# Optimization experiments

Hardware: AMD Instinct MI355X
Metric: run time of the kernel (lower is better)

## Reference

```python
import jax, jax.numpy as jnp
import numpy as np

DIM, HEADS, DHEAD, CTX_DIM, DFF = 1280, 20, 64, 768, 5120
EPS = 1e-5
SCALE = DHEAD ** -0.5


def layer_norm(x, g, b):
    mu = jnp.mean(x, axis=-1, keepdims=True)
    var = jnp.mean(jnp.square(x - mu), axis=-1, keepdims=True)
    return (x - mu) * jax.lax.rsqrt(var + EPS) * g + b


def cross_attention(x, ctx, wq, wk, wv, wo, bo):
    B, N, _ = x.shape
    M = ctx.shape[1]
    q = jnp.einsum('bne,ef->bnf', x, wq).reshape(B, N, HEADS, DHEAD).transpose(0, 2, 1, 3)
    k = jnp.einsum('bme,ef->bmf', ctx, wk).reshape(B, M, HEADS, DHEAD).transpose(0, 2, 1, 3)
    v = jnp.einsum('bme,ef->bmf', ctx, wv).reshape(B, M, HEADS, DHEAD).transpose(0, 2, 1, 3)
    scores = jnp.einsum('bhnd,bhmd->bhnm', q, k) * SCALE
    attn = jax.nn.softmax(scores, axis=-1)
    out = jnp.einsum('bhnm,bhmd->bhnd', attn, v)
    out = out.transpose(0, 2, 1, 3).reshape(B, N, HEADS * DHEAD)
    return jnp.einsum('bnf,fe->bne', out, wo) + bo


def geglu_ff(x, w1, b1, w2, b2):
    h = jnp.einsum('bne,ef->bnf', x, w1) + b1  # [B,N,2*DFF]
    a, gate = h[..., :DFF], h[..., DFF:]
    h = a * jax.nn.gelu(gate)
    return jnp.einsum('bnf,fe->bne', h, w2) + b2


def block_forward(x, context,
                  g1, be1, wq1, wk1, wv1, wo1, bo1,
                  g2, be2, wq2, wk2, wv2, wo2, bo2,
                  g3, be3, w_ff1, b_ff1, w_ff2, b_ff2):
    x = cross_attention(layer_norm(x, g1, be1), layer_norm(x, g1, be1), wq1, wk1, wv1, wo1, bo1) + x
    x = cross_attention(layer_norm(x, g2, be2), context, wq2, wk2, wv2, wo2, bo2) + x
    return geglu_ff(layer_norm(x, g3, be3), w_ff1, b_ff1, w_ff2, b_ff2) + x


def setup_inputs() -> dict:
    key = jax.random.key(0)
    ks = jax.random.split(key, 20)
    s = 0.02
    inner = HEADS * DHEAD
    return {
        'x': jax.random.normal(ks[0], (4, 1024, DIM), jnp.float32),
        'context': jax.random.normal(ks[1], (4, 77, CTX_DIM), jnp.float32),
        'g1': jnp.ones((DIM,), jnp.float32), 'be1': jnp.zeros((DIM,), jnp.float32),
        'wq1': jax.random.normal(ks[2], (DIM, inner), jnp.float32) * s,
        'wk1': jax.random.normal(ks[3], (DIM, inner), jnp.float32) * s,
        'wv1': jax.random.normal(ks[4], (DIM, inner), jnp.float32) * s,
        'wo1': jax.random.normal(ks[5], (inner, DIM), jnp.float32) * s,
        'bo1': jnp.zeros((DIM,), jnp.float32),
        'g2': jnp.ones((DIM,), jnp.float32), 'be2': jnp.zeros((DIM,), jnp.float32),
        'wq2': jax.random.normal(ks[6], (DIM, inner), jnp.float32) * s,
        'wk2': jax.random.normal(ks[7], (CTX_DIM, inner), jnp.float32) * s,
        'wv2': jax.random.normal(ks[8], (CTX_DIM, inner), jnp.float32) * s,
        'wo2': jax.random.normal(ks[9], (inner, DIM), jnp.float32) * s,
        'bo2': jnp.zeros((DIM,), jnp.float32),
        'g3': jnp.ones((DIM,), jnp.float32), 'be3': jnp.zeros((DIM,), jnp.float32),
        'w_ff1': jax.random.normal(ks[10], (DIM, 2 * DFF), jnp.float32) * s,
        'b_ff1': jnp.zeros((2 * DFF,), jnp.float32),
        'w_ff2': jax.random.normal(ks[11], (DFF, DIM), jnp.float32) * s,
        'b_ff2': jnp.zeros((DIM,), jnp.float32),
    }


def reference(x, context,
              g1, be1, wq1, wk1, wv1, wo1, bo1,
              g2, be2, wq2, wk2, wv2, wo2, bo2,
              g3, be3, w_ff1, b_ff1, w_ff2, b_ff2):
    return block_forward(x, context,
                         g1, be1, wq1, wk1, wv1, wo1, bo1,
                         g2, be2, wq2, wk2, wv2, wo2, bo2,
                         g3, be3, w_ff1, b_ff1, w_ff2, b_ff2)
```

## Files before the change

### kernel.cpp

```cpp
#include <hip/hip_runtime.h>

typedef unsigned short u16;
typedef __bf16 bf16x8 __attribute__((ext_vector_type(8)));
typedef float f32x4 __attribute__((ext_vector_type(4)));

static __device__ __forceinline__ float bf2f(u16 u) {
    union { unsigned int i; float f; } v; v.i = ((unsigned int)u) << 16; return v.f;
}
static __device__ __forceinline__ u16 f2bf(float f) {
    union { float f; unsigned int i; } v; v.f = f;
    unsigned int b = v.i;
    b += 0x7fffu + ((b >> 16) & 1u);
    return (u16)(b >> 16);
}
static __device__ __forceinline__ u16 ldbf(const void* p, size_t i, int isf32) {
    return isf32 ? f2bf(((const float*)p)[i]) : ((const u16*)p)[i];
}
static __device__ __forceinline__ float ldf(const void* p, size_t i, int isf32) {
    return isf32 ? ((const float*)p)[i] : bf2f(((const u16*)p)[i]);
}
static __device__ __forceinline__ void glds16(const u16* g, u16* l) {
    __builtin_amdgcn_global_load_lds(
        (const __attribute__((address_space(1))) unsigned int*)g,
        (__attribute__((address_space(3))) unsigned int*)l,
        16, 0, 0);
}
static __device__ __forceinline__ int xcd_swz(int lid, int nwg) {
    return ((nwg & 7) == 0) ? ((lid & 7) * (nwg >> 3) + (lid >> 3)) : lid;
}

__global__ __launch_bounds__(256) void k_detect(const u16* __restrict__ xu, int* __restrict__ flag) {
    u16 v = xu[threadIdx.x * 2];
    int e = (v >> 7) & 0xFF;
    int sane = (e >= 87 && e <= 133) ? 1 : 0;
    int total = __syncthreads_count(sane);
    if (threadIdx.x == 0) flag[0] = (total < 192) ? 1 : 0;
}

__global__ __launch_bounds__(256) void k_b2f(const void* __restrict__ in, float* __restrict__ out, int n,
                                             const int* __restrict__ flagp) {
    int isf32 = *flagp;
    int i = blockIdx.x * 256 + threadIdx.x;
    if (i < n) out[i] = ldf(in, i, isf32);
}

__global__ __launch_bounds__(256) void k_cvt(const void* __restrict__ in, u16* __restrict__ out, int n,
                                             const int* __restrict__ flagp) {
    int isf32 = *flagp;
    int i = blockIdx.x * 256 + threadIdx.x;
    if (i < n) out[i] = ldbf(in, i, isf32);
}

__global__ __launch_bounds__(256) void k_addp(float* __restrict__ X, const float* __restrict__ P, int n4) {
    int i = blockIdx.x * 256 + threadIdx.x;
    int stride = gridDim.x * 256;
    for (; i < n4; i += stride) {
        f32x4 a = ((const f32x4*)X)[i];
        f32x4 b = ((const f32x4*)P)[i];
        a[0] += b[0]; a[1] += b[1]; a[2] += b[2]; a[3] += b[3];
        ((f32x4*)X)[i] = a;
    }
}

__global__ __launch_bounds__(256) void k_transpose(const void* __restrict__ W, u16* __restrict__ Wt,
                                                   int K, int N, const int* __restrict__ flagp) {
    int isf32 = *flagp;
    __shared__ u16 T[32][33];
    int k0 = blockIdx.x * 32, n0 = blockIdx.y * 32;
    int tid = threadIdx.x;
    int c = tid & 31, rr = tid >> 5;
    #pragma unroll
    for (int j = 0; j < 4; ++j) {
        int k = rr + j * 8;
        T[k][c] = ldbf(W, (size_t)(k0 + k) * N + n0 + c, isf32);
    }
    __syncthreads();
    #pragma unroll
    for (int j = 0; j < 4; ++j) {
        int n = rr + j * 8;
        Wt[(size_t)(n0 + n) * K + k0 + c] = T[c][n];
    }
}

__global__ __launch_bounds__(256) void k_transpose3(const void* __restrict__ W0, const void* __restrict__ W1,
                                                    const void* __restrict__ W2,
                                                    u16* __restrict__ D0, u16* __restrict__ D1,
                                                    u16* __restrict__ D2,
                                                    int K, int N, const int* __restrict__ flagp) {
    int isf32 = *flagp;
    int z = blockIdx.z;
    const void* W = (z == 0) ? W0 : (z == 1) ? W1 : W2;
    u16* Wt = (z == 0) ? D0 : (z == 1) ? D1 : D2;
    __shared__ u16 T[32][33];
    int k0 = blockIdx.x * 32, n0 = blockIdx.y * 32;
    int tid = threadIdx.x;
    int c = tid & 31, rr = tid >> 5;
    #pragma unroll
    for (int j = 0; j < 4; ++j) {
        int k = rr + j * 8;
        T[k][c] = ldbf(W, (size_t)(k0 + k) * N + n0 + c, isf32);
    }
    __syncthreads();
    #pragma unroll
    for (int j = 0; j < 4; ++j) {
        int n = rr + j * 8;
        Wt[(size_t)(n0 + n) * K + k0 + c] = T[c][n];
    }
}

__global__ __launch_bounds__(256) void k_layernorm(float* __restrict__ X, const float* __restrict__ P,
                                                   const void* __restrict__ G, const void* __restrict__ Bb,
                                                   u16* __restrict__ Y, int D,
                                                   const int* __restrict__ flagp) {
    int isf32 = *flagp;
    int row = blockIdx.x;
    float* xr = X + (size_t)row * D;
    const float* pr = P ? (P + (size_t)row * D) : nullptr;
    float s = 0.f, s2 = 0.f;
    for (int i = threadIdx.x; i < D; i += 256) {
        float v = xr[i] + (P ? pr[i] : 0.f);
        s += v; s2 += v * v;
    }
    #pragma unroll
    for (int off = 32; off; off >>= 1) { s += __shfl_down(s, off); s2 += __shfl_down(s2, off); }
    __shared__ float rs[4], rs2[4];
    __shared__ float stat[2];
    int w = threadIdx.x >> 6;
    if ((threadIdx.x & 63) == 0) { rs[w] = s; rs2[w] = s2; }
    __syncthreads();
    if (threadIdx.x == 0) {
        float ts = rs[0] + rs[1] + rs[2] + rs[3];
        float ts2 = rs2[0] + rs2[1] + rs2[2] + rs2[3];
        float mu = ts / D;
        float var = ts2 / D - mu * mu;
        stat[0] = mu; stat[1] = rsqrtf(var + 1e-5f);
    }
    __syncthreads();
    float mu = stat[0], rstd = stat[1];
    u16* yr = Y + (size_t)row * D;
    for (int i = threadIdx.x; i < D; i += 256) {
        float v = xr[i] + (P ? pr[i] : 0.f);
        if (P) xr[i] = v;
        yr[i] = f2bf((v - mu) * rstd * ldf(G, i, isf32) + ldf(Bb, i, isf32));
    }
}

template <int EPI>
__global__ __launch_bounds__(512, 2) void k_gemm8(const u16* __restrict__ A, const u16* __restrict__ Bt,
                                                  void* __restrict__ Cout, const void* __restrict__ bias,
                                                  int M, int N, int K, const int* __restrict__ flagp) {
    __shared__ __align__(16) u16 sm[65536];
    const int tid = threadIdx.x;
    const int w = tid >> 6;
    const int lane = tid & 63;
    const int quad = lane >> 4, r = lane & 15;
    const int wm = w >> 2, wn = w & 3;
    const int lid = blockIdx.x + blockIdx.y * gridDim.x;
    const int nid = xcd_swz(lid, gridDim.x * gridDim.y);
    const int row0 = (nid % gridDim.x) * 256;
    const int col0 = (nid / gridDim.x) * 256;
    const int NT = K >> 6;

    const u16* aP[2][2];
    const u16* bP[2][2];
    #pragma unroll
    for (int j = 0; j < 2; ++j) {
        int c = tid + w * 64 + j * 64;
        int rj = c >> 3;
        int qe = (c & 7) ^ (rj & 7);
        #pragma unroll
        for (int h = 0; h < 2; ++h) {
            int gr = h * 128 + rj;
            aP[h][j] = A + (size_t)(row0 + gr) * K + qe * 8;
            int n = col0 + gr;
            int m = (EPI == 1) ? (((n >> 4) & 1) * 5120 + (n >> 5) * 16 + (n & 15)) : n;
            bP[h][j] = Bt + (size_t)m * K + qe * 8;
        }
    }
    auto stageA = [&](int h, int t) {
        u16* base = sm + (t & 1) * 32768 + h * 8192 + w * 1024;
        glds16(aP[h][0] + t * 64, base);
        glds16(aP[h][1] + t * 64, base + 512);
    };
    auto stageB = [&](int h, int t) {
        u16* base = sm + (t & 1) * 32768 + 16384 + h * 8192 + w * 1024;
        glds16(bP[h][0] + t * 64, base);
        glds16(bP[h][1] + t * 64, base + 512);
    };

    f32x4 acc[2][2][4][2] = {};
    const int xq = r & 7;
    bf16x8 afA[4][2], afB[4][2], bf0[2][2], bf1[2][2];

    auto readA = [&](bf16x8 (&dst)[4][2], int Ab, int half) {
        #pragma unroll
        for (int i = 0; i < 4; ++i) {
            int ar = half * 128 + wm * 64 + i * 16 + r;
            #pragma unroll
            for (int ks = 0; ks < 2; ++ks)
                dst[i][ks] = *(const bf16x8*)(sm + Ab + ar * 64 + (((ks * 4 + quad) ^ xq) * 8));
        }
    };
    auto readB = [&](bf16x8 (&dst)[2][2], int Bb, int half) {
        #pragma unroll
        for (int g = 0; g < 2; ++g) {
            int br = half * 128 + wn * 32 + g * 16 + r;
            #pragma unroll
            for (int ks = 0; ks < 2; ++ks)
                dst[g][ks] = *(const bf16x8*)(sm + Bb + br * 64 + (((ks * 4 + quad) ^ xq) * 8));
        }
    };
    auto domfma = [&](int qm, int qn, bf16x8 (&a)[4][2], bf16x8 (&b)[2][2]) {
        #pragma unroll
        for (int ks = 0; ks < 2; ++ks)
            #pragma unroll
            for (int i = 0; i < 4; ++i)
                #pragma unroll
                for (int g = 0; g < 2; ++g)
                    acc[qm][qn][i][g] = __builtin_amdgcn_mfma_f32_16x16x32_bf16(
                        a[i][ks], b[g][ks], acc[qm][qn][i][g], 0, 0, 0);
    };

    stageA(0, 0); stageB(0, 0); stageA(1, 0); stageB(1, 0);
    if (NT > 1) {
        stageA(0, 1); stageB(0, 1);
        asm volatile("s_waitcnt vmcnt(4)" ::: "memory");
    } else {
        asm volatile("s_waitcnt vmcnt(0)" ::: "memory");
    }
    __builtin_amdgcn_s_barrier();
    readA(afA, 0, 0);
    readB(bf0, 16384, 0);

    for (int t = 0; t < NT; ++t) {
        const int Ab = (t & 1) * 32768;
        const int Bb = Ab + 16384;
        const int Abn = ((t + 1) & 1) * 32768;
        readB(bf1, Bb, 1);
        __builtin_amdgcn_sched_barrier(0);
        __builtin_amdgcn_s_setprio(1);
        domfma(0, 0, afA, bf0);
        __builtin_amdgcn_s_setprio(0);
        if (t + 1 < NT) stageA(1, t + 1);
        __builtin_amdgcn_s_barrier();
        readA(afB, Ab, 1);
        __builtin_amdgcn_sched_barrier(0);
        __builtin_amdgcn_s_setprio(1);
        domfma(0, 1, afA, bf1);
        __builtin_amdgcn_s_setprio(0);
        if (t + 1 < NT) stageB(1, t + 1);
        __builtin_amdgcn_s_barrier();
        __builtin_amdgcn_s_setprio(1);
        domfma(1, 1, afB, bf1);
        __builtin_amdgcn_s_setprio(0);
        if (t + 2 < NT) stageA(0, t + 2);
        __builtin_amdgcn_s_barrier();
        __builtin_amdgcn_s_setprio(1);
        domfma(1, 0, afB, bf0);
        __builtin_amdgcn_s_setprio(0);
        if (t + 2 < NT) stageB(0, t + 2);
        if (t + 2 < NT) asm volatile("s_waitcnt vmcnt(4)" ::: "memory");
        else            asm volatile("s_waitcnt vmcnt(0)" ::: "memory");
        __builtin_amdgcn_s_barrier();
        if (t + 1 < NT) {
            readA(afA, Abn, 0);
            readB(bf0, Abn + 16384, 0);
        }
    }

    if (EPI == 0) {
        u16* C = (u16*)Cout;
        #pragma unroll
        for (int qm = 0; qm < 2; ++qm) {
            #pragma unroll
            for (int qn = 0; qn < 2; ++qn) {
                #pragma unroll
                for (int i = 0; i < 4; ++i) {
                    int grow = row0 + qm * 128 + wm * 64 + i * 16 + quad * 4;
                    #pragma unroll
                    for (int g = 0; g < 2; ++g) {
                        int gcol = col0 + qn * 128 + wn * 32 + g * 16 + r;
                        #pragma unroll
                        for (int t4 = 0; t4 < 4; ++t4)
                            C[(size_t)(grow + t4) * N + gcol] = f2bf(acc[qm][qn][i][g][t4]);
                    }
                }
            }
        }
    } else {
        const int isf32 = *flagp;
        u16* C = (u16*)Cout;
        #pragma unroll
        for (int qm = 0; qm < 2; ++qm) {
            #pragma unroll
            for (int qn = 0; qn < 2; ++qn) {
                int ncb = col0 + qn * 128 + wn * 32;
                int oc = (ncb >> 1) + r;
                float bva = ldf(bias, oc, isf32);
                float bvu = ldf(bias, 5120 + oc, isf32);
                #pragma unroll
                for (int i = 0; i < 4; ++i) {
                    int grow = row0 + qm * 128 + wm * 64 + i * 16 + quad * 4;
                    #pragma unroll
                    for (int t4 = 0; t4 < 4; ++t4) {
                        float a = acc[qm][qn][i][0][t4] + bva;
                        float u = acc[qm][qn][i][1][t4] + bvu;
                        float z2 = 1.5957691216f * (u + 0.044715f * u * u * u);
                        float gl = u * __builtin_amdgcn_rcpf(1.f + __expf(-z2));
                        C[(size_t)(grow + t4) * 5120 + oc] = f2bf(a * gl);
                    }
                }
            }
        }
    }
}

template <int EPI>
__global__ __launch_bounds__(256) void k_gemm_t(const u16* __restrict__ A, const u16* __restrict__ Bt,
                                                void* __restrict__ Cout, float* __restrict__ Rf,
                                                const void* __restrict__ bias,
                                                int M, int N, int K, const int* __restrict__ flagp) {
    int isf32 = *flagp;
    __shared__ __align__(16) u16 As[4096];
    __shared__ __align__(16) u16 Bs[4096];
    int tid = threadIdx.x;
    int row0 = blockIdx.x * 128, col0 = blockIdx.y * 128;
    int S = gridDim.z, kz = blockIdx.z;
    int kseg = K / S;
    int kb = kz * kseg, ke = kb + kseg;
    int wave = tid >> 6, lane = tid & 63;
    int wm = (wave >> 1) * 64, wn = (wave & 1) * 64;
    int quad = lane >> 4, r = lane & 15;
    int c0 = wave * 64 + lane, c1 = 256 + c0;
    int ar0 = c0 >> 2, aq0 = (c0 & 3) ^ ((ar0 >> 1) & 3);
    int ar1 = c1 >> 2, aq1 = (c1 & 3) ^ ((ar1 >> 1) & 3);
    const u16* Ag0 = A + (size_t)min(row0 + ar0, M - 1) * K + aq0 * 8;
    const u16* Ag1 = A + (size_t)min(row0 + ar1, M - 1) * K + aq1 * 8;
    const u16* Bg0 = Bt + (size_t)(col0 + ar0) * K + aq0 * 8;
    const u16* Bg1 = Bt + (size_t)(col0 + ar1) * K + aq1 * 8;
    u16* lA0 = As + wave * 512;
    u16* lA1 = As + 2048 + wave * 512;
    u16* lB0 = Bs + wave * 512;
    u16* lB1 = Bs + 2048 + wave * 512;
    f32x4 acc[4][4] = {};
    for (int k0 = kb; k0 < ke; k0 += 32) {
        __syncthreads();
        glds16(Ag0 + k0, lA0);
        glds16(Ag1 + k0, lA1);
        glds16(Bg0 + k0, lB0);
        glds16(Bg1 + k0, lB1);
        __syncthreads();
        bf16x8 af[4], bfv[4];
        #pragma unroll
        for (int i = 0; i < 4; ++i) {
            int row = wm + i * 16 + r;
            af[i] = *(const bf16x8*)(As + (row * 4 + (quad ^ ((row >> 1) & 3))) * 8);
        }
        #pragma unroll
        for (int g = 0; g < 4; ++g) {
            int row = wn + g * 16 + r;
            bfv[g] = *(const bf16x8*)(Bs + (row * 4 + (quad ^ ((row >> 1) & 3))) * 8);
        }
        #pragma unroll
        for (int i = 0; i < 4; ++i)
            #pragma unroll
            for (int g = 0; g < 4; ++g)
                acc[i][g] = __builtin_amdgcn_mfma_f32_16x16x32_bf16(af[i], bfv[g], acc[i][g], 0, 0, 0);
    }
    #pragma unroll
    for (int i = 0; i < 4; ++i) {
        int grow = row0 + wm + i * 16 + quad * 4;
        if (grow >= M) continue;
        #pragma unroll
        for (int g = 0; g < 4; ++g) {
            int gcol = col0 + wn + g * 16 + r;
            float bv = (EPI == 2 && kz == 0) ? ldf(bias, gcol, isf32) : 0.f;
            #pragma unroll
            for (int t = 0; t < 4; ++t) {
                float v = acc[i][g][t];
                size_t off = (size_t)(grow + t) * N + gcol;
                if (EPI == 0) {
                    ((u16*)Cout)[off] = f2bf(v);
                } else {
                    if (kz == 0) Rf[off] += v + bv;
                    else         ((float*)Cout)[off] = v;
                }
            }
        }
    }
}

__global__ __launch_bounds__(256) void k_geglu_t(const u16* __restrict__ A, const u16* __restrict__ Bt,
                                                 const void* __restrict__ bias, u16* __restrict__ Out,
                                                 int M, int K, const int* __restrict__ flagp) {
    const int Nout = 5120;
    int isf32 = *flagp;
    __shared__ __align__(16) u16 As[4096];
    __shared__ __align__(16) u16 Bs[4096];
    int tid = threadIdx.x;
    int row0 = blockIdx.x * 128, col0 = blockIdx.y * 64;
    int wave = tid >> 6, lane = tid & 63;
    int quad = lane >> 4, r = lane & 15;
    int c0 = wave * 64 + lane, c1 = 256 + c0;
    int ar0 = c0 >> 2, aq0 = (c0 & 3) ^ ((ar0 >> 1) & 3);
    int ar1 = c1 >> 2, aq1 = (c1 & 3) ^ ((ar1 >> 1) & 3);
    const u16* Ag0 = A + (size_t)min(row0 + ar0, M - 1) * K + aq0 * 8;
    const u16* Ag1 = A + (size_t)min(row0 + ar1, M - 1) * K + aq1 * 8;
    const u16* Bg0 = Bt + (size_t)((ar0 >> 6) * Nout + col0 + (ar0 & 63)) * K + aq0 * 8;
    const u16* Bg1 = Bt + (size_t)((ar1 >> 6) * Nout + col0 + (ar1 & 63)) * K + aq1 * 8;
    u16* lA0 = As + wave * 512;
    u16* lA1 = As + 2048 + wave * 512;
    u16* lB0 = Bs + wave * 512;
    u16* lB1 = Bs + 2048 + wave * 512;
    f32x4 acc[2][2][4] = {};
    for (int k0 = 0; k0 < K; k0 += 32) {
        __syncthreads();
        glds16(Ag0 + k0, lA0);
        glds16(Ag1 + k0, lA1);
        glds16(Bg0 + k0, lB0);
        glds16(Bg1 + k0, lB1);
        __syncthreads();
        bf16x8 af[2], bv[2][4];
        #pragma unroll
        for (int i = 0; i < 2; ++i) {
            int row = wave * 32 + i * 16 + r;
            af[i] = *(const bf16x8*)(As + (row * 4 + (quad ^ ((row >> 1) & 3))) * 8);
        }
        #pragma unroll
        for (int p = 0; p < 2; ++p)
            #pragma unroll
            for (int g = 0; g < 4; ++g) {
                int row = p * 64 + g * 16 + r;
                bv[p][g] = *(const bf16x8*)(Bs + (row * 4 + (quad ^ ((row >> 1) & 3))) * 8);
            }
        #pragma unroll
        for (int p = 0; p < 2; ++p)
            #pragma unroll
            for (int i = 0; i < 2; ++i)
                #pragma unroll
                for (int g = 0; g < 4; ++g)
                    acc[p][i][g] = __builtin_amdgcn_mfma_f32_16x16x32_bf16(af[i], bv[p][g], acc[p][i][g], 0, 0, 0);
    }
    #pragma unroll
    for (int i = 0; i < 2; ++i) {
        int grow = row0 + wave * 32 + i * 16 + quad * 4;
        #pragma unroll
        for (int g = 0; g < 4; ++g) {
            int gcol = col0 + g * 16 + r;
            float bva = ldf(bias, gcol, isf32);
            float bvu = ldf(bias, Nout + gcol, isf32);
            #pragma unroll
            for (int t = 0; t < 4; ++t) {
                float a = acc[0][i][g][t] + bva;
                float u = acc[1][i][g][t] + bvu;
                float z2 = 1.5957691216f * (u + 0.044715f * u * u * u);
                float gl = u * __builtin_amdgcn_rcpf(1.f + __expf(-z2));
                Out[(size_t)(grow + t) * Nout + gcol] = f2bf(a * gl);
            }
        }
    }
}

template <int EPI, bool AEXT>
__global__ __launch_bounds__(256) void k_gemm(const void* __restrict__ A, const void* __restrict__ B,
                                              void* __restrict__ Cout, float* __restrict__ Rf,
                                              const void* __restrict__ bias,
                                              int M, int N, int K, const int* __restrict__ flagp) {
    int isf32 = *flagp;
    __shared__ u16 As[64][40];
    __shared__ u16 Bs[64][40];
    int tid = threadIdx.x;
    int row0 = blockIdx.x * 64, col0 = blockIdx.y * 64;
    int wave = tid >> 6, lane = tid & 63;
    int wm = (wave >> 1) * 32, wn = (wave & 1) * 32;
    int quad = lane >> 4, r = lane & 15;
    int arow = tid >> 2, akk = (tid & 3) * 8;
    int bnl = tid & 63, bkk = (tid >> 6) * 8;
    int garow = row0 + arow;
    f32x4 acc[2][2] = {};
    for (int k0 = 0; k0 < K; k0 += 32) {
        uint4 aval = {0u, 0u, 0u, 0u};
        if (garow < M) {
            if (AEXT && isf32) {
                const float* Af = (const float*)A;
                u16 t[8];
                #pragma unroll
                for (int j = 0; j < 8; ++j) t[j] = f2bf(Af[(size_t)garow * K + k0 + akk + j]);
                aval = *(uint4*)t;
            } else {
                aval = *(const uint4*)((const u16*)A + (size_t)garow * K + k0 + akk);
            }
        }
        u16 btmp[8];
        #pragma unroll
        for (int j = 0; j < 8; ++j) btmp[j] = ldbf(B, (size_t)(k0 + bkk + j) * N + col0 + bnl, isf32);
        __syncthreads();
        *(uint4*)(&As[arow][akk]) = aval;
        *(uint4*)(&Bs[bnl][bkk]) = *(uint4*)btmp;
        __syncthreads();
        bf16x8 a0 = *(const bf16x8*)(&As[wm + r][quad * 8]);
        bf16x8 a1 = *(const bf16x8*)(&As[wm + 16 + r][quad * 8]);
        bf16x8 b0 = *(const bf16x8*)(&Bs[wn + r][quad * 8]);
        bf16x8 b1 = *(const bf16x8*)(&Bs[wn + 16 + r][quad * 8]);
        acc[0][0] = __builtin_amdgcn_mfma_f32_16x16x32_bf16(a0, b0, acc[0][0], 0, 0, 0);
        acc[0][1] = __builtin_amdgcn_mfma_f32_16x16x32_bf16(a0, b1, acc[0][1], 0, 0, 0);
        acc[1][0] = __builtin_amdgcn_mfma_f32_16x16x32_bf16(a1, b0, acc[1][0], 0, 0, 0);
        acc[1][1] = __builtin_amdgcn_mfma_f32_16x16x32_bf16(a1, b1, acc[1][1], 0, 0, 0);
    }
    #pragma unroll
    for (int i = 0; i < 2; ++i)
        #pragma unroll
        for (int jn = 0; jn < 2; ++jn)
            #pragma unroll
            for (int t = 0; t < 4; ++t) {
                int grow = row0 + wm + i * 16 + quad * 4 + t;
                int gcol = col0 + wn + jn * 16 + r;
                if (grow >= M) continue;
                float v = acc[i][jn][t];
                size_t off = (size_t)grow * N + gcol;
                if (EPI == 0) {
                    ((u16*)Cout)[off] = f2bf(v);
                } else if (EPI == 2) {
                    Rf[off] += v + ldf(bias, gcol, isf32);
                } else {
                    ((float*)Cout)[off] = v + ldf(bias, gcol, isf32) + Rf[off];
                }
            }
}

__global__ __launch_bounds__(256) void k_gemm_geglu(const u16* __restrict__ A, const void* __restrict__ B,
                                                    const void* __restrict__ bias, u16* __restrict__ Out,
                                                    int M, int Nout, int K, int ldb,
                                                    const int* __restrict__ flagp) {
    int isf32 = *flagp;
    __shared__ u16 As[64][40];
    __shared__ u16 Bs[64][40];
    int tid = threadIdx.x;
    int row0 = blockIdx.x * 64, col0 = blockIdx.y * 64;
    int wave = tid >> 6, lane = tid & 63;
    int wm = (wave >> 1) * 32, wn = (wave & 1) * 32;
    int quad = lane >> 4, r = lane & 15;
    int arow = tid >> 2, akk = (tid & 3) * 8;
    int bnl = tid & 63, bkk = (tid >> 6) * 8;
    int garow = row0 + arow;
    f32x4 acc[2][2][2] = {};
    for (int p = 0; p < 2; ++p) {
        for (int k0 = 0; k0 < K; k0 += 32) {
            uint4 aval = {0u, 0u, 0u, 0u};
            if (garow < M) aval = *(const uint4*)(A + (size_t)garow * K + k0 + akk);
            u16 btmp[8];
            #pragma unroll
            for (int j = 0; j < 8; ++j)
                btmp[j] = ldbf(B, (size_t)(k0 + bkk + j) * ldb + p * Nout + col0 + bnl, isf32);
            __syncthreads();
            *(uint4*)(&As[arow][akk]) = aval;
            *(uint4*)(&Bs[bnl][bkk]) = *(uint4*)btmp;
            __syncthreads();
            bf16x8 a0 = *(const bf16x8*)(&As[wm + r][quad * 8]);
            bf16x8 a1 = *(const bf16x8*)(&As[wm + 16 + r][quad * 8]);
            bf16x8 b0 = *(const bf16x8*)(&Bs[wn + r][quad * 8]);
            bf16x8 b1 = *(const bf16x8*)(&Bs[wn + 16 + r][quad * 8]);
            acc[p][0][0] = __builtin_amdgcn_mfma_f32_16x16x32_bf16(a0, b0, acc[p][0][0], 0, 0, 0);
            acc[p][0][1] = __builtin_amdgcn_mfma_f32_16x16x32_bf16(a0, b1, acc[p][0][1], 0, 0, 0);
            acc[p][1][0] = __builtin_amdgcn_mfma_f32_16x16x32_bf16(a1, b0, acc[p][1][0], 0, 0, 0);
            acc[p][1][1] = __builtin_amdgcn_mfma_f32_16x16x32_bf16(a1, b1, acc[p][1][1], 0, 0, 0);
        }
    }
    #pragma unroll
    for (int i = 0; i < 2; ++i)
        #pragma unroll
        for (int jn = 0; jn < 2; ++jn)
            #pragma unroll
            for (int t = 0; t < 4; ++t) {
                int grow = row0 + wm + i * 16 + quad * 4 + t;
                int gcol = col0 + wn + jn * 16 + r;
                if (grow >= M) continue;
                float a = acc[0][i][jn][t] + ldf(bias, gcol, isf32);
                float u = acc[1][i][jn][t] + ldf(bias, Nout + gcol, isf32);
                float th = tanhf(0.7978845608f * (u + 0.044715f * u * u * u));
                float gl = 0.5f * u * (1.f + th);
                Out[(size_t)grow * Nout + gcol] = f2bf(a * gl);
            }
}

__global__ __launch_bounds__(256) void k_attn_flash(const u16* __restrict__ Q, const u16* __restrict__ K,
                                                    const u16* __restrict__ V, u16* __restrict__ O,
                                                    int N, int Mkv, int H, int ldq, int ldkv, int ldo) {
    __shared__ u16 KT[64][72];
    __shared__ u16 VT[64][72];
    __shared__ u16 Sp[4][16][72];
    const float SC = 0.18033688f;
    int nt = N / 64;
    int qt = blockIdx.x % nt;
    int bh = blockIdx.x / nt;
    int h = bh % H, b = bh / H;
    int tid = threadIdx.x, wave = tid >> 6, lane = tid & 63;
    int quad = lane >> 4, r = lane & 15;
    int q0 = qt * 64 + wave * 16;

    const u16* qbase = Q + ((size_t)(b * N + q0 + r)) * ldq + h * 64;
    bf16x8 aq0 = *(const bf16x8*)(qbase + quad * 8);
    bf16x8 aq1 = *(const bf16x8*)(qbase + 32 + quad * 8);

    f32x4 accO[4] = {};
    float m_i = -1e30f, l_i = 0.f;

    int srow = tid >> 2;
    int scol = (tid & 3) * 8;

    for (int kv0 = 0; kv0 < Mkv; kv0 += 64) {
        int krow = min(kv0 + srow, Mkv - 1);
        const u16* kp = K + ((size_t)(b * Mkv + krow)) * ldkv + h * 64;
        const u16* vp = V + ((size_t)(b * Mkv + krow)) * ldkv + h * 64;
        uint4 ka = *(const uint4*)(kp + scol);
        uint4 kb = *(const uint4*)(kp + scol + 32);
        uint4 va = *(const uint4*)(vp + scol);
        uint4 vb = *(const uint4*)(vp + scol + 32);

        __syncthreads();
        *(uint4*)(&KT[srow][scol]) = ka;
        *(uint4*)(&KT[srow][scol + 32]) = kb;
        u16 tmp[16];
        *(uint4*)tmp = va; *(uint4*)(tmp + 8) = vb;
        #pragma unroll
        for (int j = 0; j < 8; ++j) {
            VT[scol + j][srow] = tmp[j];
            VT[scol + 32 + j][srow] = tmp[8 + j];
        }
        __syncthreads();

        bf16x8 bk[4][2];
        #pragma unroll
        for (int g = 0; g < 4; ++g) {
            bk[g][0] = *(const bf16x8*)(&KT[g * 16 + r][quad * 8]);
            bk[g][1] = *(const bf16x8*)(&KT[g * 16 + r][32 + quad * 8]);
        }
        f32x4 s[4] = {};
        #pragma unroll
        for (int g = 0; g < 4; ++g) {
            s[g] = __builtin_amdgcn_mfma_f32_16x16x32_bf16(bk[g][0], aq0, s[g], 0, 0, 0);
            s[g] = __builtin_amdgcn_mfma_f32_16x16x32_bf16(bk[g][1], aq1, s[g], 0, 0, 0);
        }

        float v[4][4];
        float vmax = -1e30f;
        #pragma unroll
        for (int g = 0; g < 4; ++g)
            #pragma unroll
            for (int t = 0; t < 4; ++t) {
                int kvi = kv0 + g * 16 + quad * 4 + t;
                v[g][t] = (kvi < Mkv) ? s[g][t] * SC : -1e30f;
                vmax = fmaxf(vmax, v[g][t]);
            }
        vmax = fmaxf(vmax, __shfl_xor(vmax, 16));
        vmax = fmaxf(vmax, __shfl_xor(vmax, 32));
        float mn = fmaxf(m_i, vmax);
        float alpha = exp2f(m_i - mn);
        float ps = 0.f;
        #pragma unroll
        for (int g = 0; g < 4; ++g)
            #pragma unroll
            for (int t = 0; t < 4; ++t) {
                v[g][t] = exp2f(v[g][t] - mn);
                ps += v[g][t];
            }
        ps += __shfl_xor(ps, 16);
        ps += __shfl_xor(ps, 32);
        l_i = l_i * alpha + ps;
        m_i = mn;
        #pragma unroll
        for (int t = 0; t < 4; ++t) {
            float art = __shfl(alpha, quad * 4 + t);
            accO[0][t] *= art; accO[1][t] *= art; accO[2][t] *= art; accO[3][t] *= art;
        }
        #pragma unroll
        for (int g = 0; g < 4; ++g)
            #pragma unroll
            for (int t = 0; t < 4; ++t)
                Sp[wave][r][g * 16 + quad * 4 + t] = f2bf(v[g][t]);

        bf16x8 ap0 = *(const bf16x8*)(&Sp[wave][r][quad * 8]);
        bf16x8 ap1 = *(const bf16x8*)(&Sp[wave][r][32 + quad * 8]);
        #pragma unroll
        for (int g = 0; g < 4; ++g) {
            bf16x8 bv0 = *(const bf16x8*)(&VT[g * 16 + r][quad * 8]);
            bf16x8 bv1 = *(const bf16x8*)(&VT[g * 16 + r][32 + quad * 8]);
            accO[g] = __builtin_amdgcn_mfma_f32_16x16x32_bf16(ap0, bv0, accO[g], 0, 0, 0);
            accO[g] = __builtin_amdgcn_mfma_f32_16x16x32_bf16(ap1, bv1, accO[g], 0, 0, 0);
        }
    }

    u16* ob = O + ((size_t)(b * N + q0)) * ldo + h * 64;
    #pragma unroll
    for (int t = 0; t < 4; ++t) {
        float lr = __shfl(l_i, quad * 4 + t);
        float inv = 1.f / lr;
        #pragma unroll
        for (int g = 0; g < 4; ++g)
            ob[(size_t)(quad * 4 + t) * ldo + g * 16 + r] = f2bf(accO[g][t] * inv);
    }
}

extern "C" void kernel_launch(void* const* d_in, const int* in_sizes, int n_in,
                              void* d_out, int out_size, void* d_ws, size_t ws_size,
                              hipStream_t stream) {
    const void* x    = d_in[0];
    const void* ctx  = d_in[1];
    const void* g1   = d_in[2];
    const void* be1  = d_in[3];
    const void* wq1  = d_in[4];
    const void* wk1  = d_in[5];
    const void* wv1  = d_in[6];
    const void* wo1  = d_in[7];
    const void* bo1  = d_in[8];
    const void* g2   = d_in[9];
    const void* be2  = d_in[10];
    const void* wq2  = d_in[11];
    const void* wk2  = d_in[12];
    const void* wv2  = d_in[13];
    const void* wo2  = d_in[14];
    const void* bo2  = d_in[15];
    const void* g3   = d_in[16];
    const void* be3  = d_in[17];
    const void* wff1 = d_in[18];
    const void* bff1 = d_in[19];
    const void* wff2 = d_in[20];
    const void* bff2 = d_in[21];

    const int BT = 4096, D = 1280;
    dim3 blk(256);
    char* ws = (char*)d_ws;

    const size_t NEED_FAST = 117393664;
    if (ws_size >= NEED_FAST) {
        int*   flag   = (int*)(ws);
        u16* lnout    = (u16*)(ws + 256);
        u16* qkv      = (u16*)(ws + 10486016);
        u16* attnout  = (u16*)(ws + 10486016 + 31457280);
        u16* gbuf     = (u16*)(ws + 10486016);
        u16* ctxb     = (u16*)(ws + 52429056);
        u16* kv2      = (u16*)(ws + 52902144);
        u16* wqkv1t   = (u16*)(ws + 54479104);
        u16* wo1t     = (u16*)(ws + 64309504);
        u16* wq2t     = (u16*)(ws + 67586304);
        u16* wkv2t    = (u16*)(ws + 70863104);
        u16* wo2t     = (u16*)(ws + 74795264);
        u16* wff1t    = (u16*)(ws + 78072064);
        u16* wff2t    = (u16*)(ws + 104286464);
        float* pff2   = (float*)(ws + 54479104);
        float* pWO    = (float*)(ws + 10486016);
        float* xres   = (float*)d_out;

        k_detect<<<dim3(1), blk, 0, stream>>>((const u16*)x, flag);
        k_b2f<<<dim3((BT * D + 255) / 256), blk, 0, stream>>>(x, xres, BT * D, flag);
        k_transpose3<<<dim3(40, 40, 3), blk, 0, stream>>>(wq1, wk1, wv1,
                                                          wqkv1t, wqkv1t + 1280 * 1280,
                                                          wqkv1t + 2 * 1280 * 1280, 1280, 1280, flag);
        k_transpose3<<<dim3(40, 40, 3), blk, 0, stream>>>(wo1, wq2, wo2,
                                                          wo1t, wq2t, wo2t, 1280, 1280, flag);
        k_transpose3<<<dim3(24, 40, 2), blk, 0, stream>>>(wk2, wv2, wv2,
                                                          wkv2t, wkv2t + 1280 * 768,
                                                          wkv2t + 1280 * 768, 768, 1280, flag);
        k_transpose<<<dim3(40, 320), blk, 0, stream>>>(wff1, wff1t, 1280, 10240, flag);
        k_transpose<<<dim3(160, 40), blk, 0, stream>>>(wff2, wff2t, 5120, 1280, flag);
        k_cvt<<<dim3((308 * 768 + 255) / 256), blk, 0, stream>>>(ctx, ctxb, 308 * 768, flag);
        k_layernorm<<<dim3(BT), blk, 0, stream>>>(xres, nullptr, g1, be1, lnout, D, flag);
        k_gemm8<0><<<dim3(16, 15), dim3(512), 0, stream>>>(lnout, wqkv1t, qkv, nullptr, BT, 3840, D, flag);
        k_attn_flash<<<dim3(16 * 80), blk, 0, stream>>>(qkv, qkv + 1280, qkv + 2560, attnout,
                                                        1024, 1024, 20, 3840, 3840, 1280);
        k_gemm_t<2><<<dim3(32, 10, 2), blk, 0, stream>>>(attnout, wo1t, pWO, xres, bo1, BT, D, D, flag);
        k_layernorm<<<dim3(BT), blk, 0, stream>>>(xres, pWO, g2, be2, lnout, D, flag);
        k_gemm_t<0><<<dim3(32, 10), blk, 0, stream>>>(lnout, wq2t, qkv, nullptr, nullptr, BT, D, D, flag);
        k_gemm_t<0><<<dim3(3, 20), blk, 0, stream>>>(ctxb, wkv2t, kv2, nullptr, nullptr, 308, 2560, 768, flag);
        k_attn_flash<<<dim3(16 * 80), blk, 0, stream>>>(qkv, kv2, kv2 + 1280, attnout,
                                                        1024, 77, 20, 1280, 2560, 1280);
        k_gemm_t<2><<<dim3(32, 10, 2), blk, 0, stream>>>(attnout, wo2t, pWO, xres, bo2, BT, D, D, flag);
        k_layernorm<<<dim3(BT), blk, 0, stream>>>(xres, pWO, g3, be3, lnout, D, flag);
        k_gemm8<1><<<dim3(16, 40), dim3(512), 0, stream>>>(lnout, wff1t, gbuf, bff1, BT, 10240, D, flag);
        k_gemm_t<2><<<dim3(32, 10, 2), blk, 0, stream>>>(gbuf, wff2t, pff2, xres, bff2, BT, D, 5120, flag);
        k_addp<<<dim3(2048), blk, 0, stream>>>(xres, pff2, BT * D / 4);
    } else {
        int*   flag    = (int*)(ws);
        float* xres    = (float*)(ws + 256);
        u16* lnout     = (u16*)(ws + 20971776);
        u16* q         = (u16*)(ws + 31457536);
        u16* kbuf      = (u16*)(ws + 41943296);
        u16* vbuf      = (u16*)(ws + 52429056);
        u16* attnout   = (u16*)(ws + 62914816);
        u16* k2        = (u16*)(ws + 73400576);
        u16* v2        = (u16*)(ws + 74189056);
        u16* gbuf      = (u16*)(ws + 31457536);

        dim3 g_gemm(64, 20);
        dim3 g_kv(5, 20);
        dim3 g_attn(16 * 80);

        k_detect<<<dim3(1), blk, 0, stream>>>((const u16*)x, flag);
        k_b2f<<<dim3((BT * D + 255) / 256), blk, 0, stream>>>(x, xres, BT * D, flag);
        k_layernorm<<<dim3(BT), blk, 0, stream>>>(xres, nullptr, g1, be1, lnout, D, flag);
        k_gemm<0, false><<<g_gemm, blk, 0, stream>>>(lnout, wq1, q, nullptr, nullptr, BT, D, D, flag);
        k_gemm<0, false><<<g_gemm, blk, 0, stream>>>(lnout, wk1, kbuf, nullptr, nullptr, BT, D, D, flag);
        k_gemm<0, false><<<g_gemm, blk, 0, stream>>>(lnout, wv1, vbuf, nullptr, nullptr, BT, D, D, flag);
        k_attn_flash<<<g_attn, blk, 0, stream>>>(q, kbuf, vbuf, attnout, 1024, 1024, 20, 1280, 1280, 1280);
        k_gemm<2, false><<<g_gemm, blk, 0, stream>>>(attnout, wo1, nullptr, xres, bo1, BT, D, D, flag);
        k_layernorm<<<dim3(BT), blk, 0, stream>>>(xres, nullptr, g2, be2, lnout, D, flag);
        k_gemm<0, false><<<g_gemm, blk, 0, stream>>>(lnout, wq2, q, nullptr, nullptr, BT, D, D, flag);
        k_gemm<0, true><<<g_kv, blk, 0, stream>>>(ctx, wk2, k2, nullptr, nullptr, 308, D, 768, flag);
        k_gemm<0, true><<<g_kv, blk, 0, stream>>>(ctx, wv2, v2, nullptr, nullptr, 308, D, 768, flag);
        k_attn_flash<<<g_attn, blk, 0, stream>>>(q, k2, v2, attnout, 1024, 77, 20, 1280, 1280, 1280);
        k_gemm<2, false><<<g_gemm, blk, 0, stream>>>(attnout, wo2, nullptr, xres, bo2, BT, D, D, flag);
        k_layernorm<<<dim3(BT), blk, 0, stream>>>(xres, nullptr, g3, be3, lnout, D, flag);
        k_gemm_geglu<<<dim3(64, 80), blk, 0, stream>>>(lnout, wff1, bff1, gbuf, BT, 5120, D, 10240, flag);
        k_gemm<3, false><<<g_gemm, blk, 0, stream>>>(gbuf, wff2, d_out, xres, bff2, BT, D, 5120, flag);
    }
}
```

Measured before the change: 776.7 us.

## Halve GEMM K-tile to 32 and target four blocks per CU

Rewrites the 256x256 bf16 GEMM mainloop to use a K-step of 32 instead of 64. This halves shared memory to 64KB and cuts fragment registers, so launch bounds can request 4 workgroups per CU instead of 2. The fine-grained four-phase ping-pong schedule with partial vmcnt waits is replaced by a simpler loop: prefetch the next tile, compute, wait for all loads, barrier. The new LDS swizzle is a rotation rather than an XOR. The cost is twice as many barriers and full waits per K, less latency hiding inside a block, and register pressure that could cause spills under the tighter bound of 128 accumulator floats per thread.

New measurement: 2.080 ms. 168% more time.

```diff
diff --git a/kernel.cpp b/kernel.cpp
--- a/kernel.cpp
+++ b/kernel.cpp
@@ -146,10 +146,10 @@
 }
 
 template <int EPI>
-__global__ __launch_bounds__(512, 2) void k_gemm8(const u16* __restrict__ A, const u16* __restrict__ Bt,
+__global__ __launch_bounds__(512, 4) void k_gemm8(const u16* __restrict__ A, const u16* __restrict__ Bt,
                                                   void* __restrict__ Cout, const void* __restrict__ bias,
                                                   int M, int N, int K, const int* __restrict__ flagp) {
-    __shared__ __align__(16) u16 sm[65536];
+    __shared__ __align__(16) u16 sm[32768];
     const int tid = threadIdx.x;
     const int w = tid >> 6;
     const int lane = tid & 63;
@@ -159,113 +159,80 @@
     const int nid = xcd_swz(lid, gridDim.x * gridDim.y);
     const int row0 = (nid % gridDim.x) * 256;
     const int col0 = (nid / gridDim.x) * 256;
-    const int NT = K >> 6;
-
-    const u16* aP[2][2];
-    const u16* bP[2][2];
+    const int NT = K >> 5;
+
+    const u16* aP[2];
+    const u16* bP[2];
     #pragma unroll
     for (int j = 0; j < 2; ++j) {
         int c = tid + w * 64 + j * 64;
-        int rj = c >> 3;
-        int qe = (c & 7) ^ (rj & 7);
-        #pragma unroll
-        for (int h = 0; h < 2; ++h) {
-            int gr = h * 128 + rj;
-            aP[h][j] = A + (size_t)(row0 + gr) * K + qe * 8;
-            int n = col0 + gr;
-            int m = (EPI == 1) ? (((n >> 4) & 1) * 5120 + (n >> 5) * 16 + (n & 15)) : n;
-            bP[h][j] = Bt + (size_t)m * K + qe * 8;
-        }
-    }
-    auto stageA = [&](int h, int t) {
-        u16* base = sm + (t & 1) * 32768 + h * 8192 + w * 1024;
-        glds16(aP[h][0] + t * 64, base);
-        glds16(aP[h][1] + t * 64, base + 512);
+        int rj = c >> 2;
+        int qs = c & 3;
+        int qe = (qs + 4 - ((rj >> 1) & 3)) & 3;
+        aP[j] = A + (size_t)(row0 + rj) * K + qe * 8;
+        int n = col0 + rj;
+        int m = (EPI == 1) ? (((n >> 4) & 1) * 5120 + (n >> 5) * 16 + (n & 15)) : n;
+        bP[j] = Bt + (size_t)m * K + qe * 8;
+    }
+    auto stage = [&](int t) {
+        u16* base = sm + (t & 1) * 16384 + w * 1024;
+        glds16(aP[0] + t * 32, base);
+        glds16(aP[1] + t * 32, base + 512);
+        glds16(bP[0] + t * 32, base + 8192);
+        glds16(bP[1] + t * 32, base + 8192 + 512);
     };
-    auto stageB = [&](int h, int t) {
-        u16* base = sm + (t & 1) * 32768 + 16384 + h * 8192 + w * 1024;
-        glds16(bP[h][0] + t * 64, base);
-        glds16(bP[h][1] + t * 64, base + 512);
-    };
 
     f32x4 acc[2][2][4][2] = {};
-    const int xq = r & 7;
-    bf16x8 afA[4][2], afB[4][2], bf0[2][2], bf1[2][2];
-
-    auto readA = [&](bf16x8 (&dst)[4][2], int Ab, int half) {
+    bf16x8 af[4], bf0[2], bf1[2];
+
+    auto readA = [&](int Ab, int half) {
         #pragma unroll
         for (int i = 0; i < 4; ++i) {
             int ar = half * 128 + wm * 64 + i * 16 + r;
-            #pragma unroll
-            for (int ks = 0; ks < 2; ++ks)
-                dst[i][ks] = *(const bf16x8*)(sm + Ab + ar * 64 + (((ks * 4 + quad) ^ xq) * 8));
+            int slot = (quad + ((ar >> 1) & 3)) & 3;
+            af[i] = *(const bf16x8*)(sm + Ab + ar * 32 + slot * 8);
         }
     };
-    auto readB = [&](bf16x8 (&dst)[2][2], int Bb, int half) {
+    auto readB = [&](bf16x8 (&dst)[2], int Ab, int half) {
         #pragma unroll
         for (int g = 0; g < 2; ++g) {
             int br = half * 128 + wn * 32 + g * 16 + r;
-            #pragma unroll
-            for (int ks = 0; ks < 2; ++ks)
-                dst[g][ks] = *(const bf16x8*)(sm + Bb + br * 64 + (((ks * 4 + quad) ^ xq) * 8));
+            int slot = (quad + ((br >> 1) & 3)) & 3;
+            dst[g] = *(const bf16x8*)(sm + Ab + 8192 + br * 32 + slot * 8);
         }
     };
-    auto domfma = [&](int qm, int qn, bf16x8 (&a)[4][2], bf16x8 (&b)[2][2]) {
-        #pragma unroll
-        for (int ks = 0; ks < 2; ++ks)
-            #pragma unroll
-            for (int i = 0; i < 4; ++i)
-                #pragma unroll
-                for (int g = 0; g < 2; ++g)
-                    acc[qm][qn][i][g] = __builtin_amdgcn_mfma_f32_16x16x32_bf16(
-                        a[i][ks], b[g][ks], acc[qm][qn][i][g], 0, 0, 0);
-    };
-
-    stageA(0, 0); stageB(0, 0); stageA(1, 0); stageB(1, 0);
-    if (NT > 1) {
-        stageA(0, 1); stageB(0, 1);
-        asm volatile("s_waitcnt vmcnt(4)" ::: "memory");
-    } else {
+
+    stage(0);
+    asm volatile("s_waitcnt vmcnt(0)" ::: "memory");
+    __builtin_amdgcn_s_barrier();
+
+    for (int t = 0; t < NT; ++t) {
+        const int Ab = (t & 1) * 16384;
+        if (t + 1 < NT) stage(t + 1);
+        readA(Ab, 0);
+        readB(bf0, Ab, 0);
+        readB(bf1, Ab, 1);
+        __builtin_amdgcn_s_setprio(1);
+        #pragma unroll
+        for (int i = 0; i < 4; ++i)
+            #pragma unroll
+            for (int g = 0; g < 2; ++g) {
+                acc[0][0][i][g] = __builtin_amdgcn_mfma_f32_16x16x32_bf16(af[i], bf0[g], acc[0][0][i][g], 0, 0, 0);
+                acc[0][1][i][g] = __builtin_amdgcn_mfma_f32_16x16x32_bf16(af[i], bf1[g], acc[0][1][i][g], 0, 0, 0);
+            }
+        __builtin_amdgcn_s_setprio(0);
+        readA(Ab, 1);
+        __builtin_amdgcn_s_setprio(1);
+        #pragma unroll
+        for (int i = 0; i < 4; ++i)
+            #pragma unroll
+            for (int g = 0; g < 2; ++g) {
+                acc[1][0][i][g] = __builtin_amdgcn_mfma_f32_16x16x32_bf16(af[i], bf0[g], acc[1][0][i][g], 0, 0, 0);
+                acc[1][1][i][g] = __builtin_amdgcn_mfma_f32_16x16x32_bf16(af[i], bf1[g], acc[1][1][i][g], 0, 0, 0);
+            }
+        __builtin_amdgcn_s_setprio(0);
         asm volatile("s_waitcnt vmcnt(0)" ::: "memory");
-    }
-    __builtin_amdgcn_s_barrier();
-    readA(afA, 0, 0);
-    readB(bf0, 16384, 0);
-
-    for (int t = 0; t < NT; ++t) {
-        const int Ab = (t & 1) * 32768;
-        const int Bb = Ab + 16384;
-        const int Abn = ((t + 1) & 1) * 32768;
-        readB(bf1, Bb, 1);
-        __builtin_amdgcn_sched_barrier(0);
-        __builtin_amdgcn_s_setprio(1);
-        domfma(0, 0, afA, bf0);
-        __builtin_amdgcn_s_setprio(0);
-        if (t + 1 < NT) stageA(1, t + 1);
         __builtin_amdgcn_s_barrier();
-        readA(afB, Ab, 1);
-        __builtin_amdgcn_sched_barrier(0);
-        __builtin_amdgcn_s_setprio(1);
-        domfma(0, 1, afA, bf1);
-        __builtin_amdgcn_s_setprio(0);
-        if (t + 1 < NT) stageB(1, t + 1);
-        __builtin_amdgcn_s_barrier();
-        __builtin_amdgcn_s_setprio(1);
-        domfma(1, 1, afB, bf1);
-        __builtin_amdgcn_s_setprio(0);
-        if (t + 2 < NT) stageA(0, t + 2);
-        __builtin_amdgcn_s_barrier();
-        __builtin_amdgcn_s_setprio(1);
-        domfma(1, 0, afB, bf0);
-        __builtin_amdgcn_s_setprio(0);
-        if (t + 2 < NT) stageB(0, t + 2);
-        if (t + 2 < NT) asm volatile("s_waitcnt vmcnt(4)" ::: "memory");
-        else            asm volatile("s_waitcnt vmcnt(0)" ::: "memory");
-        __builtin_amdgcn_s_barrier();
-        if (t + 1 < NT) {
-            readA(afA, Abn, 0);
-            readB(bf0, Abn + 16384, 0);
-        }
     }
 
     if (EPI == 0) {
```
